# Kernel optimization log

Measured on AMD Instinct MI355X. Metric: run time of the kernel, lower is better.

The kernel has to match this reference:

```python
import jax, jax.numpy as jnp
import numpy as np

B, D, O = 16384, 1024, 1024
NUM_TASKS = 2
E = 4  # experts per group (2 task groups + 1 shared group)


def setup_inputs() -> dict:
    key = jax.random.key(0)
    ks = jax.random.split(key, 7)
    x = jax.random.normal(ks[0], (B, D), dtype=jnp.float32)
    # Stacked expert params: groups g in {task0, task1, shared}, each with E experts.
    W = jax.random.normal(ks[1], (3, E, D, O), dtype=jnp.float32) * 0.02  # Linear weight (in,out layout)
    b = jax.random.normal(ks[2], (3, E, O), dtype=jnp.float32) * 0.02
    # Per-task gates over (E specific + E shared) = 8 experts.
    Wg = jax.random.normal(ks[3], (NUM_TASKS, D, 2 * E), dtype=jnp.float32) * 0.02
    bg = jax.random.normal(ks[4], (NUM_TASKS, 2 * E), dtype=jnp.float32) * 0.02
    # Shared gate over all 3*E = 12 experts (is_top=False).
    Wgs = jax.random.normal(ks[5], (D, 3 * E), dtype=jnp.float32) * 0.02
    bgs = jax.random.normal(ks[6], (3 * E,), dtype=jnp.float32) * 0.02
    return {"x": x, "W": W, "b": b, "Wg": Wg, "bg": bg, "Wgs": Wgs, "bgs": bgs}


def reference(x, W, b, Wg, bg, Wgs, bgs):
    # All 12 experts share the same input (single-input branch): one batched GEMM.
    # h: [3, B, E, O]  (dropout is identity in eval mode)
    h = jax.nn.relu(jnp.einsum('bd,gedo->gbeo', x, W) + b[:, None, :, :])
    # Per-task gates: [T, B, 2E]
    sel_t = jax.nn.softmax(jnp.einsum('bd,tdm->tbm', x, Wg) + bg[:, None, :], axis=-1)
    outs = []
    for t in range(NUM_TASKS):
        mat = jnp.concatenate([h[t], h[2]], axis=1)  # [B, 2E, O]
        outs.append(jnp.einsum('bmo,bm->bo', mat, sel_t[t]))
    # Shared gate over all experts (is_top=False): [B, 3E]
    sel_s = jax.nn.softmax(x @ Wgs + bgs, axis=-1)
    mat_all = jnp.concatenate([h[0], h[1], h[2]], axis=1)  # [B, 3E, O]
    outs.append(jnp.einsum('bmo,bm->bo', mat_all, sel_s))
    return tuple(outs)
```

## Files before the change

### kernel.cpp

```cpp
#include <hip/hip_runtime.h>

typedef unsigned short ushort_t;
typedef __attribute__((ext_vector_type(8))) short short8;
typedef __attribute__((ext_vector_type(4))) float floatx4;

#define B_ROWS 16384
#define BO 16777216
#define MC 4096

__device__ __forceinline__ ushort_t f2bf(float f){
  unsigned u = __float_as_uint(f);
  u += 0x7fffu + ((u >> 16) & 1u);
  return (ushort_t)(u >> 16);
}
__device__ __forceinline__ float bf2f(ushort_t u){
  return __uint_as_float(((unsigned)u) << 16);
}

__device__ __forceinline__ void gld_lds16(void* l, const void* g){
  __builtin_amdgcn_global_load_lds(
      (__attribute__((address_space(1))) void*)(g),
      (__attribute__((address_space(3))) void*)(l), 16, 0, 0);
}

__global__ void cvt_x(const float* __restrict__ x, ushort_t* __restrict__ xb){
  const int i = (blockIdx.x * 256 + threadIdx.x) * 4;
  const floatx4 v = *(const floatx4*)(x + i);
  ushort4 o;
  o.x = f2bf(v[0]); o.y = f2bf(v[1]); o.z = f2bf(v[2]); o.w = f2bf(v[3]);
  *(ushort4*)(xb + i) = o;
}

__global__ void cvt_wt(const float* __restrict__ W, ushort_t* __restrict__ wt){
  __shared__ float t[64][65];
  const int blk = blockIdx.x;
  const int ge = blk >> 8, dt = (blk >> 4) & 15, ot = blk & 15;
  const float* src = W + ((size_t)ge << 20) + (size_t)(dt * 64) * 1024 + ot * 64;
  const int c4 = (threadIdx.x & 15) * 4, r0 = threadIdx.x >> 4;
#pragma unroll
  for (int p = 0; p < 4; ++p){
    const int r = r0 + p * 16;
    const floatx4 v = *(const floatx4*)(src + (size_t)r * 1024 + c4);
    t[r][c4] = v[0]; t[r][c4+1] = v[1]; t[r][c4+2] = v[2]; t[r][c4+3] = v[3];
  }
  __syncthreads();
  ushort_t* dst = wt + ((size_t)ge << 20) + (size_t)(ot * 64) * 1024 + dt * 64;
  const int d4 = (threadIdx.x & 15) * 4, o0 = threadIdx.x >> 4;
#pragma unroll
  for (int p = 0; p < 4; ++p){
    const int o = o0 + p * 16;
    ushort4 ov;
    ov.x = f2bf(t[d4][o]);   ov.y = f2bf(t[d4+1][o]);
    ov.z = f2bf(t[d4+2][o]); ov.w = f2bf(t[d4+3][o]);
    *(ushort4*)(dst + (size_t)o * 1024 + d4) = ov;
  }
}

__global__ void cvt_wg(const float* __restrict__ Wg, const float* __restrict__ bg,
                       const float* __restrict__ Wgs, const float* __restrict__ bgs,
                       ushort_t* __restrict__ wgcat, float* __restrict__ biascat){
  const int m = blockIdx.x;
#pragma unroll
  for (int j = 0; j < 4; ++j){
    const int d = j * 256 + threadIdx.x;
    float v;
    if (m < 16)      v = Wg[((size_t)((m >> 3) * 1024 + d)) * 8 + (m & 7)];
    else if (m < 28) v = Wgs[(size_t)d * 12 + (m - 16)];
    else             v = 0.f;
    wgcat[m * 1024 + d] = f2bf(v);
  }
  if (threadIdx.x == 0){
    float bv;
    if (m < 16)      bv = bg[m];
    else if (m < 28) bv = bgs[m - 16];
    else             bv = -1e30f;
    biascat[m] = bv;
  }
}

__global__ __launch_bounds__(256) void gates_mfma(
    const ushort_t* __restrict__ xb, const ushort_t* __restrict__ wgcat,
    const float* __restrict__ biascat, float* __restrict__ selT)
{
  __shared__ __align__(16) char gsm[20480];
  const int tid = threadIdx.x;
  const int lane = tid & 63;
  const int w = tid >> 6;
  const int lr = lane & 15;
  const int brow = blockIdx.x * 128;

  const int sc = (((tid & 7) ^ ((tid >> 3) & 7)) << 4);
  const char* aS = (const char*)xb + (size_t)(brow + (tid >> 3)) * 2048 + sc;
  const char* bS = (const char*)wgcat + (size_t)(tid >> 3) * 2048 + sc;

  const int kx0 = (((lane >> 4) << 4)) ^ ((lane & 7) << 4);
  const int kx1 = (64 + ((lane >> 4) << 4)) ^ ((lane & 7) << 4);

  int aOff[2], bOff[2];
#pragma unroll
  for (int m = 0; m < 2; ++m) aOff[m] = (w * 32 + m * 16 + lr) * 128;
#pragma unroll
  for (int n = 0; n < 2; ++n) bOff[n] = 16384 + (n * 16 + lr) * 128;

  const floatx4 fz = {0.f, 0.f, 0.f, 0.f};
  floatx4 hacc[2][2];
#pragma unroll
  for (int m = 0; m < 2; ++m)
#pragma unroll
    for (int n = 0; n < 2; ++n) hacc[m][n] = fz;

  for (int kt = 0; kt < 16; ++kt){
    const size_t ko = (size_t)kt * 128;
#pragma unroll
    for (int j = 0; j < 4; ++j)
      gld_lds16(gsm + j * 4096 + w * 1024, aS + (size_t)j * 65536 + ko);
    gld_lds16(gsm + 16384 + w * 1024, bS + ko);
    __syncthreads();
    short8 av[2][2], bv[2][2];
#pragma unroll
    for (int m = 0; m < 2; ++m){
      av[m][0] = *(const short8*)(gsm + aOff[m] + kx0);
      av[m][1] = *(const short8*)(gsm + aOff[m] + kx1);
    }
#pragma unroll
    for (int n = 0; n < 2; ++n){
      bv[n][0] = *(const short8*)(gsm + bOff[n] + kx0);
      bv[n][1] = *(const short8*)(gsm + bOff[n] + kx1);
    }
#pragma unroll
    for (int m = 0; m < 2; ++m)
#pragma unroll
      for (int n = 0; n < 2; ++n){
        hacc[m][n] = __builtin_amdgcn_mfma_f32_16x16x32_bf16(av[m][0], bv[n][0], hacc[m][n], 0, 0, 0);
        hacc[m][n] = __builtin_amdgcn_mfma_f32_16x16x32_bf16(av[m][1], bv[n][1], hacc[m][n], 0, 0, 0);
      }
    __syncthreads();
  }

  const float bc0 = biascat[lr];
  const float bc1 = biascat[16 + lr];
#pragma unroll
  for (int m = 0; m < 2; ++m){
#pragma unroll
    for (int r = 0; r < 4; ++r){
      float l0 = hacc[m][0][r] + bc0;
      float l1 = hacc[m][1][r] + bc1;
      float mx0 = l0;
#pragma unroll
      for (int s = 1; s < 8; s <<= 1) mx0 = fmaxf(mx0, __shfl_xor(mx0, s, 64));
      float e0 = __expf(l0 - mx0);
      float s0 = e0;
#pragma unroll
      for (int s = 1; s < 8; s <<= 1) s0 += __shfl_xor(s0, s, 64);
      float mx1 = l1;
#pragma unroll
      for (int s = 1; s < 16; s <<= 1) mx1 = fmaxf(mx1, __shfl_xor(mx1, s, 64));
      float e1 = __expf(l1 - mx1);
      float s1 = e1;
#pragma unroll
      for (int s = 1; s < 16; s <<= 1) s1 += __shfl_xor(s1, s, 64);
      const int row = brow + w * 32 + m * 16 + ((lane >> 4) << 2) + r;
      selT[(size_t)lr * B_ROWS + row] = e0 / s0;
      if (lr < 12) selT[(size_t)(16 + lr) * B_ROWS + row] = e1 / s1;
    }
  }
}

__global__ __launch_bounds__(512, 2) void pass1_gemm(
    const ushort_t* __restrict__ xb,
    const ushort_t* __restrict__ wt,
    const float* __restrict__ bias,
    ushort_t* __restrict__ h,
    int chunk_row0)
{
  __shared__ __align__(16) char smem[131072];
  const int tid  = threadIdx.x;
  const int lane = tid & 63;
  const int wv   = tid >> 6;
  const int wm   = wv >> 2;
  const int wn   = wv & 3;
  const int lr   = lane & 15;
  const int NT   = 48;

  const int bid = blockIdx.x;
  const int L = (bid & 7) * 32 + (bid >> 3);
  const int eg = L >> 6;
  const int nt = (L >> 4) & 3;
  const int mt = L & 15;
  const int brow_l = mt * 256;
  const int browg  = chunk_row0 + brow_l;
  const int bcol   = nt * 256;

  const int sc = (((tid & 7) ^ ((tid >> 3) & 7)) << 4);
  const char* aSrc[2];
  size_t bOffBase[2];
#pragma unroll
  for (int hh = 0; hh < 2; ++hh){
    aSrc[hh] = (const char*)xb + (size_t)(browg + hh * 128 + (tid >> 3)) * 2048 + sc;
    bOffBase[hh] = (size_t)(bcol + hh * 128 + (tid >> 3)) * 2048 + sc;
  }

  auto stageA = [&](int hh, int kt, int bo){
    char* d = smem + bo + hh * 16384 + wv * 1024;
    const char* s = aSrc[hh] + (size_t)(kt & 15) * 128;
    gld_lds16(d, s);
    gld_lds16(d + 8192, s + 131072);
  };
  auto stageB = [&](int hh, int kt, int bo){
    const int exk = eg * 3 + (kt >> 4);
    char* d = smem + bo + 32768 + hh * 16384 + wv * 1024;
    const char* s = (const char*)wt + ((size_t)exk << 21) + bOffBase[hh]
                  + (size_t)(kt & 15) * 128;
    gld_lds16(d, s);
    gld_lds16(d + 8192, s + 131072);
  };

  const int kx0 = (((lane >> 4) << 4)) ^ ((lane & 7) << 4);
  const int kx1 = (64 + ((lane >> 4) << 4)) ^ ((lane & 7) << 4);
  int aOff[8], bOff[4];
#pragma unroll
  for (int m = 0; m < 8; ++m) aOff[m] = wm * 16384 + (m * 16 + lr) * 128;
#pragma unroll
  for (int n = 0; n < 4; ++n)
    bOff[n] = 32768 + (wn >> 1) * 16384 + ((wn & 1) * 64 + n * 16 + lr) * 128;

  const floatx4 fz = {0.f, 0.f, 0.f, 0.f};
  floatx4 hacc[8][4];
#pragma unroll
  for (int m = 0; m < 8; ++m)
#pragma unroll
    for (int n = 0; n < 4; ++n) hacc[m][n] = fz;

  const int colw = bcol + wn * 64;
  const int g4 = (lane >> 4) << 2;
  auto EPI = [&](int el){
    const int exk = eg * 3 + el;
    ushort_t* hbase = h + ((size_t)exk * MC) * 1024;
    floatx4 bv[4];
#pragma unroll
    for (int n = 0; n < 4; ++n)
      bv[n] = *(const floatx4*)(bias + exk * 1024 + colw + n * 16 + g4);
#pragma unroll
    for (int m = 0; m < 8; ++m){
      const int row = brow_l + wm * 128 + m * 16 + lr;
      ushort_t* hp = hbase + (size_t)row * 1024 + colw + g4;
#pragma unroll
      for (int n = 0; n < 4; ++n){
        const float v0 = fmaxf(hacc[m][n][0] + bv[n][0], 0.f);
        const float v1 = fmaxf(hacc[m][n][1] + bv[n][1], 0.f);
        const float v2 = fmaxf(hacc[m][n][2] + bv[n][2], 0.f);
        const float v3 = fmaxf(hacc[m][n][3] + bv[n][3], 0.f);
        uint2 pk;
        pk.x = (unsigned)f2bf(v0) | ((unsigned)f2bf(v1) << 16);
        pk.y = (unsigned)f2bf(v2) | ((unsigned)f2bf(v3) << 16);
        *(uint2*)(hp + n * 16) = pk;
        hacc[m][n] = fz;
      }
    }
  };

  stageA(0, 0, 0); stageA(1, 0, 0); stageB(0, 0, 0); stageB(1, 0, 0);
  stageB(0, 1, 65536); stageA(0, 1, 65536); stageA(1, 1, 65536);
  asm volatile("s_waitcnt vmcnt(6)" ::: "memory");
  __builtin_amdgcn_s_barrier();

#define LDF(X) (*(const short8*)(smem + (X)))
#define MFMA_(A, Bv, C) __builtin_amdgcn_mfma_f32_16x16x32_bf16(A, Bv, C, 0, 0, 0)
#define LGKM0_SB() { asm volatile("s_waitcnt lgkmcnt(0)" ::: "memory"); __builtin_amdgcn_sched_barrier(0); }

  for (int i = 0; i < NT; ++i){
    const int cur = (i & 1) << 16;
    const int nxt = cur ^ 65536;

    short8 a0[4][2], b0[2][2];
#pragma unroll
    for (int m = 0; m < 4; ++m){
      a0[m][0] = LDF(cur + aOff[m] + kx0);
      a0[m][1] = LDF(cur + aOff[m] + kx1);
    }
#pragma unroll
    for (int n = 0; n < 2; ++n){
      b0[n][0] = LDF(cur + bOff[n] + kx0);
      b0[n][1] = LDF(cur + bOff[n] + kx1);
    }
    if (i + 1 < NT) stageB(1, i + 1, nxt);
    __builtin_amdgcn_s_barrier();
    LGKM0_SB();
    __builtin_amdgcn_s_setprio(1);
#pragma unroll
    for (int m = 0; m < 4; ++m)
#pragma unroll
      for (int n = 0; n < 2; ++n){
        hacc[m][n] = MFMA_(b0[n][0], a0[m][0], hacc[m][n]);
        hacc[m][n] = MFMA_(b0[n][1], a0[m][1], hacc[m][n]);
      }
    __builtin_amdgcn_s_setprio(0);
    __builtin_amdgcn_s_barrier();

    short8 b1[2][2];
#pragma unroll
    for (int n = 0; n < 2; ++n){
      b1[n][0] = LDF(cur + bOff[2 + n] + kx0);
      b1[n][1] = LDF(cur + bOff[2 + n] + kx1);
    }
    __builtin_amdgcn_s_barrier();
    LGKM0_SB();
    __builtin_amdgcn_s_setprio(1);
#pragma unroll
    for (int m = 0; m < 4; ++m)
#pragma unroll
      for (int n = 0; n < 2; ++n){
        hacc[m][2 + n] = MFMA_(b1[n][0], a0[m][0], hacc[m][2 + n]);
        hacc[m][2 + n] = MFMA_(b1[n][1], a0[m][1], hacc[m][2 + n]);
      }
    __builtin_amdgcn_s_setprio(0);
    __builtin_amdgcn_s_barrier();

    short8 a1[4][2];
#pragma unroll
    for (int m = 0; m < 4; ++m){
      a1[m][0] = LDF(cur + aOff[4 + m] + kx0);
      a1[m][1] = LDF(cur + aOff[4 + m] + kx1);
    }
    if (i + 2 < NT) stageB(0, i + 2, cur);
    __builtin_amdgcn_s_barrier();
    LGKM0_SB();
    __builtin_amdgcn_s_setprio(1);
#pragma unroll
    for (int m = 0; m < 4; ++m)
#pragma unroll
      for (int n = 0; n < 2; ++n){
        hacc[4 + m][n] = MFMA_(b0[n][0], a1[m][0], hacc[4 + m][n]);
        hacc[4 + m][n] = MFMA_(b0[n][1], a1[m][1], hacc[4 + m][n]);
      }
    __builtin_amdgcn_s_setprio(0);
    __builtin_amdgcn_s_barrier();

    if (i + 2 < NT) { stageA(0, i + 2, cur); stageA(1, i + 2, cur); }
    __builtin_amdgcn_s_barrier();
    __builtin_amdgcn_s_setprio(1);
#pragma unroll
    for (int m = 0; m < 4; ++m)
#pragma unroll
      for (int n = 0; n < 2; ++n){
        hacc[4 + m][2 + n] = MFMA_(b1[n][0], a1[m][0], hacc[4 + m][2 + n]);
        hacc[4 + m][2 + n] = MFMA_(b1[n][1], a1[m][1], hacc[4 + m][2 + n]);
      }
    __builtin_amdgcn_s_setprio(0);
    if ((i & 15) == 15) EPI(i >> 4);
    if ((i & 15) == 15 && i < NT - 2)      { asm volatile("s_waitcnt vmcnt(38)" ::: "memory"); }
    else if (i < NT - 2)                   { asm volatile("s_waitcnt vmcnt(6)"  ::: "memory"); }
    else if (i == NT - 2)                  { asm volatile("s_waitcnt vmcnt(0)"  ::: "memory"); }
    __builtin_amdgcn_s_barrier();
  }
#undef LDF
#undef MFMA_
#undef LGKM0_SB
}

__global__ __launch_bounds__(256) void combine_kernel(
    const ushort_t* __restrict__ h,
    const float* __restrict__ selT,
    float* __restrict__ out,
    int row0)
{
  const int tid = threadIdx.x;
  const int lb  = blockIdx.x * 2 + (tid >> 7);
  const int b   = row0 + lb;
  const int c   = (tid & 127) * 8;
  const ushort_t* hp = h + (size_t)lb * 1024 + c;

  float a0[8], a1[8], as_[8];
#pragma unroll
  for (int k = 0; k < 8; ++k){ a0[k] = 0.f; a1[k] = 0.f; as_[k] = 0.f; }

#pragma unroll
  for (int e = 0; e < 4; ++e){
    const float w0 = selT[(size_t)e * B_ROWS + b];
    const float ws = selT[(size_t)(16 + e) * B_ROWS + b];
    const short8 hv = *(const short8*)(hp + (size_t)e * (MC * 1024));
#pragma unroll
    for (int k = 0; k < 8; ++k){
      const float f = bf2f((ushort_t)hv[k]);
      a0[k] += w0 * f; as_[k] += ws * f;
    }
  }
#pragma unroll
  for (int e = 0; e < 4; ++e){
    const float w1 = selT[(size_t)(8 + e) * B_ROWS + b];
    const float ws = selT[(size_t)(20 + e) * B_ROWS + b];
    const short8 hv = *(const short8*)(hp + (size_t)(4 + e) * (MC * 1024));
#pragma unroll
    for (int k = 0; k < 8; ++k){
      const float f = bf2f((ushort_t)hv[k]);
      a1[k] += w1 * f; as_[k] += ws * f;
    }
  }
#pragma unroll
  for (int e = 0; e < 4; ++e){
    const float w0 = selT[(size_t)(4 + e) * B_ROWS + b];
    const float w1 = selT[(size_t)(12 + e) * B_ROWS + b];
    const float ws = selT[(size_t)(24 + e) * B_ROWS + b];
    const short8 hv = *(const short8*)(hp + (size_t)(8 + e) * (MC * 1024));
#pragma unroll
    for (int k = 0; k < 8; ++k){
      const float f = bf2f((ushort_t)hv[k]);
      a0[k] += w0 * f; a1[k] += w1 * f; as_[k] += ws * f;
    }
  }

  float* o0 = out + (size_t)b * 1024 + c;
  *(floatx4*)(o0)     = *(const floatx4*)(a0);
  *(floatx4*)(o0 + 4) = *(const floatx4*)(a0 + 4);
  float* o1 = o0 + BO;
  *(floatx4*)(o1)     = *(const floatx4*)(a1);
  *(floatx4*)(o1 + 4) = *(const floatx4*)(a1 + 4);
  float* o2 = o1 + BO;
  *(floatx4*)(o2)     = *(const floatx4*)(as_);
  *(floatx4*)(o2 + 4) = *(const floatx4*)(as_ + 4);
}

__global__ void gates_kernel(const float* __restrict__ x,
                             const float* __restrict__ Wg,
                             const float* __restrict__ bg,
                             const float* __restrict__ Wgs,
                             const float* __restrict__ bgs,
                             float* __restrict__ selT)
{
  const int lane = threadIdx.x & 63;
  const int w    = threadIdx.x >> 6;
  const int b    = blockIdx.x * 4 + w;
  const float* xr = x + (size_t)b * 1024;
  float acc[28];
#pragma unroll
  for (int m = 0; m < 28; ++m) acc[m] = 0.f;
#pragma unroll
  for (int j = 0; j < 4; ++j){
    const int d0 = (j * 64 + lane) * 4;
    const floatx4 xv = *(const floatx4*)(xr + d0);
#pragma unroll
    for (int q = 0; q < 4; ++q){
      const float xs = xv[q];
      const int d = d0 + q;
      const float* g0 = Wg + d * 8;
      const float* g1 = Wg + 8192 + d * 8;
      const float* gs = Wgs + d * 12;
#pragma unroll
      for (int m = 0; m < 8; ++m)  acc[m]      += xs * g0[m];
#pragma unroll
      for (int m = 0; m < 8; ++m)  acc[8 + m]  += xs * g1[m];
#pragma unroll
      for (int m = 0; m < 12; ++m) acc[16 + m] += xs * gs[m];
    }
  }
#pragma unroll
  for (int m = 0; m < 28; ++m){
    float v = acc[m];
#pragma unroll
    for (int off = 1; off < 64; off <<= 1) v += __shfl_xor(v, off, 64);
    acc[m] = v;
  }
  if (lane == 0){
    float e0[8], e1[8], es[12];
    float mx0 = -1e30f, mx1 = -1e30f, mxs = -1e30f;
#pragma unroll
    for (int m = 0; m < 8; ++m){  e0[m] = acc[m]      + bg[m];     mx0 = fmaxf(mx0, e0[m]); }
#pragma unroll
    for (int m = 0; m < 8; ++m){  e1[m] = acc[8 + m]  + bg[8 + m]; mx1 = fmaxf(mx1, e1[m]); }
#pragma unroll
    for (int m = 0; m < 12; ++m){ es[m] = acc[16 + m] + bgs[m];    mxs = fmaxf(mxs, es[m]); }
    float s0 = 0.f, s1 = 0.f, ss = 0.f;
#pragma unroll
    for (int m = 0; m < 8; ++m){  e0[m] = __expf(e0[m] - mx0); s0 += e0[m]; }
#pragma unroll
    for (int m = 0; m < 8; ++m){  e1[m] = __expf(e1[m] - mx1); s1 += e1[m]; }
#pragma unroll
    for (int m = 0; m < 12; ++m){ es[m] = __expf(es[m] - mxs); ss += es[m]; }
    const float r0 = 1.f / s0, r1 = 1.f / s1, rs = 1.f / ss;
#pragma unroll
    for (int m = 0; m < 8; ++m)  selT[(size_t)m * B_ROWS + b]        = e0[m] * r0;
#pragma unroll
    for (int m = 0; m < 8; ++m)  selT[(size_t)(8 + m) * B_ROWS + b]  = e1[m] * r1;
#pragma unroll
    for (int m = 0; m < 12; ++m) selT[(size_t)(16 + m) * B_ROWS + b] = es[m] * rs;
  }
}

__global__ __launch_bounds__(256, 2) void moe_kernel(
    const ushort_t* __restrict__ xb,
    const ushort_t* __restrict__ wt,
    const float* __restrict__ bias,
    const float* __restrict__ selT,
    float* __restrict__ out)
{
  __shared__ __align__(16) char smem[24576];
  const int tid  = threadIdx.x;
  const int lane = tid & 63;
  const int wid  = tid >> 6;
  const int wm   = wid >> 1;
  const int wn   = wid & 1;
  const int brow = (blockIdx.x >> 4) << 7;
  const int bcol = (blockIdx.x & 15) << 6;
  const int rstg = tid >> 3;
  const int scol = ((tid & 7) << 4) ^ ((rstg & 7) << 4);
  size_t aoff[4], boff[2];
#pragma unroll
  for (int i = 0; i < 4; ++i) aoff[i] = (size_t)(brow + i * 32 + rstg) * 2048 + scol;
#pragma unroll
  for (int i = 0; i < 2; ++i) boff[i] = (size_t)(bcol + i * 32 + rstg) * 2048 + scol;
  char* aldst = smem + wid * 1024;
  char* bldst = smem + 16384 + wid * 1024;
  const int kl   = (lane >> 4) << 4;
  const int swzr = (lane & 7) << 4;
  int arow[4], brw[2];
#pragma unroll
  for (int m = 0; m < 4; ++m) arow[m] = (wm * 64 + m * 16 + (lane & 15)) * 128;
#pragma unroll
  for (int n = 0; n < 2; ++n) brw[n] = 16384 + (wn * 32 + n * 16 + (lane & 15)) * 128;
  const floatx4 fz = {0.f, 0.f, 0.f, 0.f};
  floatx4 o0a[4][2], o1a[4][2], osa[4][2];
#pragma unroll
  for (int m = 0; m < 4; ++m)
#pragma unroll
    for (int n = 0; n < 2; ++n){ o0a[m][n] = fz; o1a[m][n] = fz; osa[m][n] = fz; }
  const int c0 = bcol + wn * 32 + (lane & 15);
  const int rb = brow + wm * 64 + ((lane >> 4) << 2);
  for (int ex = 0; ex < 12; ++ex){
    floatx4 hacc[4][2];
#pragma unroll
    for (int m = 0; m < 4; ++m)
#pragma unroll
      for (int n = 0; n < 2; ++n) hacc[m][n] = fz;
    const size_t wbase = (size_t)ex << 21;
    for (int kt = 0; kt < 16; ++kt){
      const size_t ko = (size_t)kt << 7;
#pragma unroll
      for (int i = 0; i < 4; ++i)
        gld_lds16(aldst + i * 4096, (const char*)xb + aoff[i] + ko);
#pragma unroll
      for (int i = 0; i < 2; ++i)
        gld_lds16(bldst + i * 4096, (const char*)wt + wbase + boff[i] + ko);
      __syncthreads();
#pragma unroll
      for (int kk = 0; kk < 2; ++kk){
        short8 av[4], bv[2];
        const int kb = (kk << 6) + kl;
#pragma unroll
        for (int m = 0; m < 4; ++m)
          av[m] = *(const short8*)(smem + arow[m] + (kb ^ swzr));
#pragma unroll
        for (int n = 0; n < 2; ++n)
          bv[n] = *(const short8*)(smem + brw[n] + (kb ^ swzr));
#pragma unroll
        for (int m = 0; m < 4; ++m)
#pragma unroll
          for (int n = 0; n < 2; ++n)
            hacc[m][n] = __builtin_amdgcn_mfma_f32_16x16x32_bf16(av[m], bv[n], hacc[m][n], 0, 0, 0);
      }
      __syncthreads();
    }
    const int g = ex >> 2, e = ex & 3;
    const float bi0 = bias[ex * 1024 + c0];
    const float bi1 = bias[ex * 1024 + c0 + 16];
    int i0, i1, is_;
    if (g == 0)      { i0 = e;     i1 = -1;     is_ = 16 + e; }
    else if (g == 1) { i0 = -1;    i1 = 8 + e;  is_ = 20 + e; }
    else             { i0 = 4 + e; i1 = 12 + e; is_ = 24 + e; }
#pragma unroll
    for (int m = 0; m < 4; ++m){
      const int rg = rb + m * 16;
      const floatx4 wsv = *(const floatx4*)(selT + (size_t)is_ * B_ROWS + rg);
      floatx4 w0 = fz, w1 = fz;
      if (i0 >= 0) w0 = *(const floatx4*)(selT + (size_t)i0 * B_ROWS + rg);
      if (i1 >= 0) w1 = *(const floatx4*)(selT + (size_t)i1 * B_ROWS + rg);
#pragma unroll
      for (int n = 0; n < 2; ++n){
        const float bi = n ? bi1 : bi0;
#pragma unroll
        for (int r = 0; r < 4; ++r){
          float hv = hacc[m][n][r] + bi;
          hv = fmaxf(hv, 0.f);
          osa[m][n][r] += wsv[r] * hv;
          o0a[m][n][r] += w0[r] * hv;
          o1a[m][n][r] += w1[r] * hv;
        }
      }
    }
  }
#pragma unroll
  for (int m = 0; m < 4; ++m){
#pragma unroll
    for (int n = 0; n < 2; ++n){
#pragma unroll
      for (int r = 0; r < 4; ++r){
        const size_t idx = (size_t)(rb + m * 16 + r) * 1024 + (c0 + (n << 4));
        out[idx]          = o0a[m][n][r];
        out[idx + BO]     = o1a[m][n][r];
        out[idx + 2 * BO] = osa[m][n][r];
      }
    }
  }
}

extern "C" void kernel_launch(void* const* d_in, const int* in_sizes, int n_in,
                              void* d_out, int out_size, void* d_ws, size_t ws_size,
                              hipStream_t stream) {
  const float* x   = (const float*)d_in[0];
  const float* W   = (const float*)d_in[1];
  const float* b   = (const float*)d_in[2];
  const float* Wg  = (const float*)d_in[3];
  const float* bg  = (const float*)d_in[4];
  const float* Wgs = (const float*)d_in[5];
  const float* bgs = (const float*)d_in[6];
  float* out = (float*)d_out;

  char* ws = (char*)d_ws;
  ushort_t* xb   = (ushort_t*)ws;
  ushort_t* wtp  = (ushort_t*)(ws + 33554432);
  float*    selT = (float*)(ws + 58720256);
  ushort_t* wgc  = (ushort_t*)(ws + 60555264);
  float*    bcat = (float*)(ws + 60620800);
  ushort_t* hbuf = (ushort_t*)(ws + 67108864);

  const bool two_pass = ws_size >= (size_t)(67108864 + 12 * MC * 1024 * 2);

  cvt_x<<<dim3(16384), dim3(256), 0, stream>>>(x, xb);
  cvt_wt<<<dim3(3072), dim3(256), 0, stream>>>(W, wtp);

  if (two_pass){
    cvt_wg<<<dim3(32), dim3(256), 0, stream>>>(Wg, bg, Wgs, bgs, wgc, bcat);
    gates_mfma<<<dim3(128), dim3(256), 0, stream>>>(xb, wgc, bcat, selT);
    for (int c = 0; c < 16384 / MC; ++c){
      pass1_gemm<<<dim3(256), dim3(512), 0, stream>>>(xb, wtp, b, hbuf, c * MC);
      combine_kernel<<<dim3(MC / 2), dim3(256), 0, stream>>>(hbuf, selT, out, c * MC);
    }
  } else {
    gates_kernel<<<dim3(4096), dim3(256), 0, stream>>>(x, Wg, bg, Wgs, bgs, selT);
    moe_kernel<<<dim3(2048), dim3(256), 0, stream>>>(xb, wtp, b, selT, out);
  }
}
```

Before: 615.5 us.

## Restructure GEMM main loop into two MFMA phases with register-prefetched fragments

Reorganizes the expert GEMM inner loop from four barrier-separated MFMA phases down to two. The next tile's A and B fragments are preloaded into registers at the end of each iteration, and the global-to-LDS staging schedule and vmcnt wait counts are changed to match. The aim is to cut barriers and lgkmcnt stalls so that LDS reads overlap with MFMA work. In exchange it raises register pressure and depends on hand-tuned wait counts, which could create hazards if they are wrong.

```diff
diff --git a/kernel.cpp b/kernel.cpp
--- a/kernel.cpp
+++ b/kernel.cpp
@@ -259,103 +259,94 @@
     }
   };
 
-  stageA(0, 0, 0); stageA(1, 0, 0); stageB(0, 0, 0); stageB(1, 0, 0);
-  stageB(0, 1, 65536); stageA(0, 1, 65536); stageA(1, 1, 65536);
-  asm volatile("s_waitcnt vmcnt(6)" ::: "memory");
-  __builtin_amdgcn_s_barrier();
-
 #define LDF(X) (*(const short8*)(smem + (X)))
 #define MFMA_(A, Bv, C) __builtin_amdgcn_mfma_f32_16x16x32_bf16(A, Bv, C, 0, 0, 0)
-#define LGKM0_SB() { asm volatile("s_waitcnt lgkmcnt(0)" ::: "memory"); __builtin_amdgcn_sched_barrier(0); }
+
+  stageA(0, 0, 0); stageA(1, 0, 0); stageB(0, 0, 0); stageB(1, 0, 0);
+  stageB(0, 1, 65536);
+  asm volatile("s_waitcnt vmcnt(2)" ::: "memory");
+  __builtin_amdgcn_s_barrier();
+  __builtin_amdgcn_sched_barrier(0);
+
+  short8 a0[4][2], b0[2][2], b1[2][2];
+#pragma unroll
+  for (int m = 0; m < 4; ++m){
+    a0[m][0] = LDF(aOff[m] + kx0);
+    a0[m][1] = LDF(aOff[m] + kx1);
+  }
+#pragma unroll
+  for (int n = 0; n < 2; ++n){
+    b0[n][0] = LDF(bOff[n] + kx0);
+    b0[n][1] = LDF(bOff[n] + kx1);
+    b1[n][0] = LDF(bOff[2 + n] + kx0);
+    b1[n][1] = LDF(bOff[2 + n] + kx1);
+  }
 
   for (int i = 0; i < NT; ++i){
     const int cur = (i & 1) << 16;
     const int nxt = cur ^ 65536;
 
-    short8 a0[4][2], b0[2][2];
-#pragma unroll
-    for (int m = 0; m < 4; ++m){
-      a0[m][0] = LDF(cur + aOff[m] + kx0);
-      a0[m][1] = LDF(cur + aOff[m] + kx1);
-    }
-#pragma unroll
-    for (int n = 0; n < 2; ++n){
-      b0[n][0] = LDF(cur + bOff[n] + kx0);
-      b0[n][1] = LDF(cur + bOff[n] + kx1);
-    }
-    if (i + 1 < NT) stageB(1, i + 1, nxt);
-    __builtin_amdgcn_s_barrier();
-    LGKM0_SB();
-    __builtin_amdgcn_s_setprio(1);
-#pragma unroll
-    for (int m = 0; m < 4; ++m)
-#pragma unroll
-      for (int n = 0; n < 2; ++n){
-        hacc[m][n] = MFMA_(b0[n][0], a0[m][0], hacc[m][n]);
-        hacc[m][n] = MFMA_(b0[n][1], a0[m][1], hacc[m][n]);
-      }
-    __builtin_amdgcn_s_setprio(0);
-    __builtin_amdgcn_s_barrier();
-
-    short8 b1[2][2];
-#pragma unroll
-    for (int n = 0; n < 2; ++n){
-      b1[n][0] = LDF(cur + bOff[2 + n] + kx0);
-      b1[n][1] = LDF(cur + bOff[2 + n] + kx1);
-    }
-    __builtin_amdgcn_s_barrier();
-    LGKM0_SB();
-    __builtin_amdgcn_s_setprio(1);
-#pragma unroll
-    for (int m = 0; m < 4; ++m)
-#pragma unroll
-      for (int n = 0; n < 2; ++n){
-        hacc[m][2 + n] = MFMA_(b1[n][0], a0[m][0], hacc[m][2 + n]);
-        hacc[m][2 + n] = MFMA_(b1[n][1], a0[m][1], hacc[m][2 + n]);
-      }
-    __builtin_amdgcn_s_setprio(0);
-    __builtin_amdgcn_s_barrier();
-
     short8 a1[4][2];
 #pragma unroll
     for (int m = 0; m < 4; ++m){
       a1[m][0] = LDF(cur + aOff[4 + m] + kx0);
       a1[m][1] = LDF(cur + aOff[4 + m] + kx1);
     }
-    if (i + 2 < NT) stageB(0, i + 2, cur);
-    __builtin_amdgcn_s_barrier();
-    LGKM0_SB();
+    if (i + 1 < NT){ stageA(0, i + 1, nxt); stageA(1, i + 1, nxt); stageB(1, i + 1, nxt); }
+    __builtin_amdgcn_sched_barrier(0);
     __builtin_amdgcn_s_setprio(1);
 #pragma unroll
     for (int m = 0; m < 4; ++m)
 #pragma unroll
       for (int n = 0; n < 2; ++n){
-        hacc[4 + m][n] = MFMA_(b0[n][0], a1[m][0], hacc[4 + m][n]);
-        hacc[4 + m][n] = MFMA_(b0[n][1], a1[m][1], hacc[4 + m][n]);
+        hacc[m][n]     = MFMA_(b0[n][0], a0[m][0], hacc[m][n]);
+        hacc[m][n]     = MFMA_(b0[n][1], a0[m][1], hacc[m][n]);
+        hacc[m][2 + n] = MFMA_(b1[n][0], a0[m][0], hacc[m][2 + n]);
+        hacc[m][2 + n] = MFMA_(b1[n][1], a0[m][1], hacc[m][2 + n]);
       }
     __builtin_amdgcn_s_setprio(0);
     __builtin_amdgcn_s_barrier();
 
-    if (i + 2 < NT) { stageA(0, i + 2, cur); stageA(1, i + 2, cur); }
-    __builtin_amdgcn_s_barrier();
+    if (i + 2 < NT) stageB(0, i + 2, cur);
+    __builtin_amdgcn_sched_barrier(0);
     __builtin_amdgcn_s_setprio(1);
 #pragma unroll
     for (int m = 0; m < 4; ++m)
 #pragma unroll
       for (int n = 0; n < 2; ++n){
+        hacc[4 + m][n]     = MFMA_(b0[n][0], a1[m][0], hacc[4 + m][n]);
+        hacc[4 + m][n]     = MFMA_(b0[n][1], a1[m][1], hacc[4 + m][n]);
         hacc[4 + m][2 + n] = MFMA_(b1[n][0], a1[m][0], hacc[4 + m][2 + n]);
         hacc[4 + m][2 + n] = MFMA_(b1[n][1], a1[m][1], hacc[4 + m][2 + n]);
       }
     __builtin_amdgcn_s_setprio(0);
     if ((i & 15) == 15) EPI(i >> 4);
-    if ((i & 15) == 15 && i < NT - 2)      { asm volatile("s_waitcnt vmcnt(38)" ::: "memory"); }
-    else if (i < NT - 2)                   { asm volatile("s_waitcnt vmcnt(6)"  ::: "memory"); }
-    else if (i == NT - 2)                  { asm volatile("s_waitcnt vmcnt(0)"  ::: "memory"); }
-    __builtin_amdgcn_s_barrier();
+
+    if (i < NT - 2){
+      if ((i & 15) == 15) { asm volatile("s_waitcnt vmcnt(34)" ::: "memory"); }
+      else                { asm volatile("s_waitcnt vmcnt(2)"  ::: "memory"); }
+    } else if (i == NT - 2){
+      asm volatile("s_waitcnt vmcnt(0)" ::: "memory");
+    }
+    if (i + 1 < NT){
+      __builtin_amdgcn_s_barrier();
+      __builtin_amdgcn_sched_barrier(0);
+#pragma unroll
+      for (int m = 0; m < 4; ++m){
+        a0[m][0] = LDF(nxt + aOff[m] + kx0);
+        a0[m][1] = LDF(nxt + aOff[m] + kx1);
+      }
+#pragma unroll
+      for (int n = 0; n < 2; ++n){
+        b0[n][0] = LDF(nxt + bOff[n] + kx0);
+        b0[n][1] = LDF(nxt + bOff[n] + kx1);
+        b1[n][0] = LDF(nxt + bOff[2 + n] + kx0);
+        b1[n][1] = LDF(nxt + bOff[2 + n] + kx1);
+      }
+    }
   }
 #undef LDF
 #undef MFMA_
-#undef LGKM0_SB
 }
 
 __global__ __launch_bounds__(256) void combine_kernel(
```

New measurement: 683.2 us. 11.0% more time.

## Restructure GEMM main loop into two-step unrolled A/B split double buffer

Applied to the files above, without the earlier changes.

Rearranges shared memory so the A tiles of both buffers sit in the first 64KB and the B tiles in the second 64KB. The main loop is unrolled by two k-steps with fixed buffer offsets, and the prefetch of the next tiles is interleaved differently across the MFMA phases, with adjusted vmcnt waits. The goal is to remove the runtime buffer-offset arithmetic and to spread global-to-LDS loads more evenly across the compute phases. In exchange the code is larger, and the hand-tuned wait counts become a new correctness risk.

```diff
diff --git a/kernel.cpp b/kernel.cpp
--- a/kernel.cpp
+++ b/kernel.cpp
@@ -200,15 +200,15 @@
     bOffBase[hh] = (size_t)(bcol + hh * 128 + (tid >> 3)) * 2048 + sc;
   }
 
-  auto stageA = [&](int hh, int kt, int bo){
-    char* d = smem + bo + hh * 16384 + wv * 1024;
+  auto stageA = [&](int hh, int kt, int buf){
+    char* d = smem + buf + hh * 16384 + wv * 1024;
     const char* s = aSrc[hh] + (size_t)(kt & 15) * 128;
     gld_lds16(d, s);
     gld_lds16(d + 8192, s + 131072);
   };
-  auto stageB = [&](int hh, int kt, int bo){
+  auto stageB = [&](int hh, int kt, int buf){
     const int exk = eg * 3 + (kt >> 4);
-    char* d = smem + bo + 32768 + hh * 16384 + wv * 1024;
+    char* d = smem + 65536 + buf + hh * 16384 + wv * 1024;
     const char* s = (const char*)wt + ((size_t)exk << 21) + bOffBase[hh]
                   + (size_t)(kt & 15) * 128;
     gld_lds16(d, s);
@@ -222,7 +222,7 @@
   for (int m = 0; m < 8; ++m) aOff[m] = wm * 16384 + (m * 16 + lr) * 128;
 #pragma unroll
   for (int n = 0; n < 4; ++n)
-    bOff[n] = 32768 + (wn >> 1) * 16384 + ((wn & 1) * 64 + n * 16 + lr) * 128;
+    bOff[n] = 65536 + (wn >> 1) * 16384 + ((wn & 1) * 64 + n * 16 + lr) * 128;
 
   const floatx4 fz = {0.f, 0.f, 0.f, 0.f};
   floatx4 hacc[8][4];
@@ -259,31 +259,31 @@
     }
   };
 
-  stageA(0, 0, 0); stageA(1, 0, 0); stageB(0, 0, 0); stageB(1, 0, 0);
-  stageB(0, 1, 65536); stageA(0, 1, 65536); stageA(1, 1, 65536);
-  asm volatile("s_waitcnt vmcnt(6)" ::: "memory");
-  __builtin_amdgcn_s_barrier();
-
 #define LDF(X) (*(const short8*)(smem + (X)))
 #define MFMA_(A, Bv, C) __builtin_amdgcn_mfma_f32_16x16x32_bf16(A, Bv, C, 0, 0, 0)
 #define LGKM0_SB() { asm volatile("s_waitcnt lgkmcnt(0)" ::: "memory"); __builtin_amdgcn_sched_barrier(0); }
 
-  for (int i = 0; i < NT; ++i){
-    const int cur = (i & 1) << 16;
-    const int nxt = cur ^ 65536;
-
-    short8 a0[4][2], b0[2][2];
+  stageA(0, 0, 0); stageA(1, 0, 0); stageB(0, 0, 0); stageB(1, 0, 0);
+  stageA(0, 1, 32768); stageA(1, 1, 32768);
+  asm volatile("s_waitcnt vmcnt(4)" ::: "memory");
+  __builtin_amdgcn_s_barrier();
+
+  for (int j = 0; j < 24; ++j){
+    const int t = 2 * j;
+
+    short8 a0[4][2], a1[4][2], b0[2][2], b1[2][2];
+
 #pragma unroll
     for (int m = 0; m < 4; ++m){
-      a0[m][0] = LDF(cur + aOff[m] + kx0);
-      a0[m][1] = LDF(cur + aOff[m] + kx1);
+      a0[m][0] = LDF(aOff[m] + kx0);
+      a0[m][1] = LDF(aOff[m] + kx1);
     }
 #pragma unroll
     for (int n = 0; n < 2; ++n){
-      b0[n][0] = LDF(cur + bOff[n] + kx0);
-      b0[n][1] = LDF(cur + bOff[n] + kx1);
-    }
-    if (i + 1 < NT) stageB(1, i + 1, nxt);
+      b0[n][0] = LDF(bOff[n] + kx0);
+      b0[n][1] = LDF(bOff[n] + kx1);
+    }
+    stageB(0, t + 1, 32768);
     __builtin_amdgcn_s_barrier();
     LGKM0_SB();
     __builtin_amdgcn_s_setprio(1);
@@ -297,12 +297,12 @@
     __builtin_amdgcn_s_setprio(0);
     __builtin_amdgcn_s_barrier();
 
-    short8 b1[2][2];
-#pragma unroll
-    for (int n = 0; n < 2; ++n){
-      b1[n][0] = LDF(cur + bOff[2 + n] + kx0);
-      b1[n][1] = LDF(cur + bOff[2 + n] + kx1);
-    }
+#pragma unroll
+    for (int m = 0; m < 4; ++m){
+      a1[m][0] = LDF(aOff[4 + m] + kx0);
+      a1[m][1] = LDF(aOff[4 + m] + kx1);
+    }
+    stageB(1, t + 1, 32768);
     __builtin_amdgcn_s_barrier();
     LGKM0_SB();
     __builtin_amdgcn_s_setprio(1);
@@ -310,19 +310,57 @@
     for (int m = 0; m < 4; ++m)
 #pragma unroll
       for (int n = 0; n < 2; ++n){
+        hacc[4 + m][n] = MFMA_(b0[n][0], a1[m][0], hacc[4 + m][n]);
+        hacc[4 + m][n] = MFMA_(b0[n][1], a1[m][1], hacc[4 + m][n]);
+      }
+    __builtin_amdgcn_s_setprio(0);
+    __builtin_amdgcn_s_barrier();
+
+#pragma unroll
+    for (int n = 0; n < 2; ++n){
+      b1[n][0] = LDF(bOff[2 + n] + kx0);
+      b1[n][1] = LDF(bOff[2 + n] + kx1);
+    }
+    if (t + 2 < NT) stageA(0, t + 2, 0);
+    __builtin_amdgcn_s_barrier();
+    LGKM0_SB();
+    __builtin_amdgcn_s_setprio(1);
+#pragma unroll
+    for (int m = 0; m < 4; ++m)
+#pragma unroll
+      for (int n = 0; n < 2; ++n){
         hacc[m][2 + n] = MFMA_(b1[n][0], a0[m][0], hacc[m][2 + n]);
         hacc[m][2 + n] = MFMA_(b1[n][1], a0[m][1], hacc[m][2 + n]);
       }
     __builtin_amdgcn_s_setprio(0);
     __builtin_amdgcn_s_barrier();
 
-    short8 a1[4][2];
+    if (t + 2 < NT) stageA(1, t + 2, 0);
+    __builtin_amdgcn_s_barrier();
+    __builtin_amdgcn_s_setprio(1);
+#pragma unroll
+    for (int m = 0; m < 4; ++m)
+#pragma unroll
+      for (int n = 0; n < 2; ++n){
+        hacc[4 + m][2 + n] = MFMA_(b1[n][0], a1[m][0], hacc[4 + m][2 + n]);
+        hacc[4 + m][2 + n] = MFMA_(b1[n][1], a1[m][1], hacc[4 + m][2 + n]);
+      }
+    __builtin_amdgcn_s_setprio(0);
+    if (t + 2 < NT) { asm volatile("s_waitcnt vmcnt(4)" ::: "memory"); }
+    else            { asm volatile("s_waitcnt vmcnt(0)" ::: "memory"); }
+    __builtin_amdgcn_s_barrier();
+
 #pragma unroll
     for (int m = 0; m < 4; ++m){
-      a1[m][0] = LDF(cur + aOff[4 + m] + kx0);
-      a1[m][1] = LDF(cur + aOff[4 + m] + kx1);
-    }
-    if (i + 2 < NT) stageB(0, i + 2, cur);
+      a0[m][0] = LDF(32768 + aOff[m] + kx0);
+      a0[m][1] = LDF(32768 + aOff[m] + kx1);
+    }
+#pragma unroll
+    for (int n = 0; n < 2; ++n){
+      b0[n][0] = LDF(32768 + bOff[n] + kx0);
+      b0[n][1] = LDF(32768 + bOff[n] + kx1);
+    }
+    if (t + 2 < NT) stageB(0, t + 2, 0);
     __builtin_amdgcn_s_barrier();
     LGKM0_SB();
     __builtin_amdgcn_s_setprio(1);
@@ -330,13 +368,51 @@
     for (int m = 0; m < 4; ++m)
 #pragma unroll
       for (int n = 0; n < 2; ++n){
+        hacc[m][n] = MFMA_(b0[n][0], a0[m][0], hacc[m][n]);
+        hacc[m][n] = MFMA_(b0[n][1], a0[m][1], hacc[m][n]);
+      }
+    __builtin_amdgcn_s_setprio(0);
+    __builtin_amdgcn_s_barrier();
+
+#pragma unroll
+    for (int m = 0; m < 4; ++m){
+      a1[m][0] = LDF(32768 + aOff[4 + m] + kx0);
+      a1[m][1] = LDF(32768 + aOff[4 + m] + kx1);
+    }
+    if (t + 2 < NT) stageB(1, t + 2, 0);
+    __builtin_amdgcn_s_barrier();
+    LGKM0_SB();
+    __builtin_amdgcn_s_setprio(1);
+#pragma unroll
+    for (int m = 0; m < 4; ++m)
+#pragma unroll
+      for (int n = 0; n < 2; ++n){
         hacc[4 + m][n] = MFMA_(b0[n][0], a1[m][0], hacc[4 + m][n]);
         hacc[4 + m][n] = MFMA_(b0[n][1], a1[m][1], hacc[4 + m][n]);
       }
     __builtin_amdgcn_s_setprio(0);
     __builtin_amdgcn_s_barrier();
 
-    if (i + 2 < NT) { stageA(0, i + 2, cur); stageA(1, i + 2, cur); }
+#pragma unroll
+    for (int n = 0; n < 2; ++n){
+      b1[n][0] = LDF(32768 + bOff[2 + n] + kx0);
+      b1[n][1] = LDF(32768 + bOff[2 + n] + kx1);
+    }
+    if (t + 3 < NT) stageA(0, t + 3, 32768);
+    __builtin_amdgcn_s_barrier();
+    LGKM0_SB();
+    __builtin_amdgcn_s_setprio(1);
+#pragma unroll
+    for (int m = 0; m < 4; ++m)
+#pragma unroll
+      for (int n = 0; n < 2; ++n){
+        hacc[m][2 + n] = MFMA_(b1[n][0], a0[m][0], hacc[m][2 + n]);
+        hacc[m][2 + n] = MFMA_(b1[n][1], a0[m][1], hacc[m][2 + n]);
+      }
+    __builtin_amdgcn_s_setprio(0);
+    __builtin_amdgcn_s_barrier();
+
+    if (t + 3 < NT) stageA(1, t + 3, 32768);
     __builtin_amdgcn_s_barrier();
     __builtin_amdgcn_s_setprio(1);
 #pragma unroll
@@ -347,11 +423,12 @@
         hacc[4 + m][2 + n] = MFMA_(b1[n][1], a1[m][1], hacc[4 + m][2 + n]);
       }
     __builtin_amdgcn_s_setprio(0);
-    if ((i & 15) == 15) EPI(i >> 4);
-    if ((i & 15) == 15 && i < NT - 2)      { asm volatile("s_waitcnt vmcnt(38)" ::: "memory"); }
-    else if (i < NT - 2)                   { asm volatile("s_waitcnt vmcnt(6)"  ::: "memory"); }
-    else if (i == NT - 2)                  { asm volatile("s_waitcnt vmcnt(0)"  ::: "memory"); }
-    __builtin_amdgcn_s_barrier();
+    if ((j & 7) == 7) EPI(j >> 3);
+    if (t + 2 < NT){
+      if ((j & 7) == 7) { asm volatile("s_waitcnt vmcnt(36)" ::: "memory"); }
+      else              { asm volatile("s_waitcnt vmcnt(4)"  ::: "memory"); }
+      __builtin_amdgcn_s_barrier();
+    }
   }
 #undef LDF
 #undef MFMA_
```

New measurement: 632.8 us. 1.03x slower.
